# Performance work log

Hardware: AMD Instinct MI355X
Metric: run time of the kernel (lower is better)

The kernel has to match this reference:

```python
import jax, jax.numpy as jnp
import numpy as np

FS = 128; WIN = 4; C_IN = 64; C_OUT = 512; BATCH = 1024
K = FS // 4            # conv kernel = 32
STRIDE = K // 2        # 16
WS = FS * WIN          # 512 samples
T = (WS - K) // STRIDE + 1  # 31 time steps
THRESH = 1.0
BN_EPS = 1e-5

# snntorch-style spike with ATan surrogate (alpha=2): fwd Heaviside, bwd 1/(1+(pi*x)^2)
@jax.custom_vjp
def spike_fn(x):
    return (x > 0).astype(x.dtype)

def _spike_fwd(x):
    return (x > 0).astype(x.dtype), x

def _spike_bwd(x, g):
    return (g / (1.0 + (jnp.pi * x) ** 2),)

spike_fn.defvjp(_spike_fwd, _spike_bwd)

def leaky_step(inp, mem, beta):
    # snntorch Leaky, reset_mechanism='subtract': reset computed from PREVIOUS mem, detached
    reset = jax.lax.stop_gradient((mem > THRESH).astype(mem.dtype))
    mem_new = jnp.clip(beta, 0.0, 1.0) * mem + inp - reset * THRESH
    spk = spike_fn(mem_new - THRESH)
    return spk, mem_new

def setup_inputs() -> dict:
    key = jax.random.key(0)
    ks = jax.random.split(key, 10)
    return {
        "x": jax.random.normal(ks[0], (BATCH, C_IN, WS), jnp.float32),
        "conv_w": jax.random.normal(ks[1], (C_OUT, C_IN, K), jnp.float32) * (1.0 / np.sqrt(C_IN * K)),
        "conv_b": jax.random.normal(ks[2], (C_OUT,), jnp.float32) * 0.01,
        "bn_gamma": jnp.ones((C_OUT,), jnp.float32),
        "bn_beta": jnp.zeros((C_OUT,), jnp.float32),
        "bn_mean": jnp.zeros((C_OUT,), jnp.float32),
        "bn_var": jnp.ones((C_OUT,), jnp.float32),
        "fc1_w": jax.random.normal(ks[3], (C_OUT, C_OUT), jnp.float32) * (1.0 / np.sqrt(C_OUT)),
        "fc1_b": jax.random.normal(ks[4], (C_OUT,), jnp.float32) * 0.01,
        "fc2_w": jax.random.normal(ks[5], (2, C_OUT), jnp.float32) * (1.0 / np.sqrt(C_OUT)),
        "fc2_b": jax.random.normal(ks[6], (2,), jnp.float32) * 0.01,
        "beta_enc": jax.random.uniform(ks[7], (C_OUT,), jnp.float32),
        "beta_hid": jax.random.uniform(ks[8], (C_OUT,), jnp.float32),
        "beta_out": jax.random.uniform(ks[9], (2,), jnp.float32),
    }

def reference(x, conv_w, conv_b, bn_gamma, bn_beta, bn_mean, bn_var,
              fc1_w, fc1_b, fc2_w, fc2_b, beta_enc, beta_hid, beta_out):
    # Conv1d: x [B, C_in, WS] -> [B, C_out, T]
    out = jax.lax.conv_general_dilated(
        x, conv_w, window_strides=(STRIDE,), padding='VALID',
        dimension_numbers=('NCH', 'OIH', 'NCH')) + conv_b[None, :, None]
    # BatchNorm1d (eval mode with running stats); dropout is identity in eval
    inv = jax.lax.rsqrt(bn_var + BN_EPS)
    out = bn_gamma[None, :, None] * (out - bn_mean[None, :, None]) * inv[None, :, None] + bn_beta[None, :, None]
    seq = jnp.transpose(out, (2, 0, 1))  # [T, B, C_out]

    mems0 = (jnp.zeros((BATCH, C_OUT), out.dtype),
             jnp.zeros((BATCH, C_OUT), out.dtype),
             jnp.zeros((BATCH, 2), out.dtype))

    def step(carry, xt):
        em, hm, om = carry
        spk_e, em = leaky_step(xt, em, beta_enc)
        cur1 = spk_e @ fc1_w.T + fc1_b
        spk_h, hm = leaky_step(cur1, hm, beta_hid)
        cur2 = spk_h @ fc2_w.T + fc2_b
        spk_o, om = leaky_step(cur2, om, beta_out)
        return (em, hm, om), (spk_o, om)

    (em, hm, om), (spk_rec, mem_rec) = jax.lax.scan(step, mems0, seq)
    return om, spk_rec, mem_rec
```

## Files before the change

### kernel.cpp

```cpp
#include <hip/hip_runtime.h>

#define T_STEPS 31
#define CIN     64
#define COUT    512
#define WSLEN   512
#define CSTRIDE 16
#define KRED    2048
#define NBATCH  1024
#define BCHUNK  512
#define MCHUNK  (BCHUNK * T_STEPS)
#define NMT     (MCHUNK / 16)

typedef int v4i __attribute__((ext_vector_type(4)));

__device__ __forceinline__ double clip01d(double v) { return fmin(fmax(v, 0.0), 1.0); }

__device__ __forceinline__ void gl_lds16(const void* g, void* l) {
    __builtin_amdgcn_global_load_lds(
        (const __attribute__((address_space(1))) void*)g,
        (__attribute__((address_space(3))) void*)l, 16, 0, 0);
}

__device__ __forceinline__ void dig5(float4 f, unsigned int w[5]) {
    float vv[4] = {f.x, f.y, f.z, f.w};
    unsigned int w0 = 0, w1 = 0, w2 = 0, w3 = 0, w4 = 0;
    #pragma unroll
    for (int e = 0; e < 4; ++e) {
        float v  = vv[e];
        float c0 = rintf(v * 16384.0f);
        float r1 = fmaf(c0, -6.103515625e-05f, v);
        float c1 = rintf(r1 * 268435456.0f);
        float r2 = fmaf(c1, -3.725290298461914e-09f, r1);
        float c2 = rintf(r2 * 34359738368.0f);
        int i0 = (int)c0, i1 = (int)c1, i2 = (int)c2;
        int d2 = ((i0 + 64) & 127) - 64;
        int d1 = (i0 - d2) >> 7;
        int d4 = ((i1 + 64) & 127) - 64;
        int d3 = (i1 - d4) >> 7;
        w0 |= (unsigned int)(d1 & 255) << (8 * e);
        w1 |= (unsigned int)(d2 & 255) << (8 * e);
        w2 |= (unsigned int)(d3 & 255) << (8 * e);
        w3 |= (unsigned int)(d4 & 255) << (8 * e);
        w4 |= (unsigned int)(i2 & 255) << (8 * e);
    }
    w[0] = w0; w[1] = w1; w[2] = w2; w[3] = w3; w[4] = w4;
}

__global__ __launch_bounds__(256) void prep_digits_kernel(
    const float* __restrict__ conv_w, const float* __restrict__ fc1_w,
    signed char* __restrict__ Bd, signed char* __restrict__ Fd)
{
    int t = blockIdx.x * 256 + threadIdx.x;
    if (t < 262144) {
        int k4 = (t & 511) << 2;
        int co = t >> 9;
        float4 w4 = *(const float4*)(conv_w + (size_t)co * KRED + k4);
        float4 v4 = make_float4(w4.x * 4.0f, w4.y * 4.0f, w4.z * 4.0f, w4.w * 4.0f);
        unsigned int pk[5];
        dig5(v4, pk);
        int off = (((k4 >> 6) * 32 + (co >> 4)) << 10)
                + ((co & 15) + ((k4 >> 4) & 3) * 16) * 16 + (k4 & 15);
        #pragma unroll
        for (int q = 0; q < 5; ++q)
            *(unsigned int*)(Bd + q * 1048576 + off) = pk[q];
    } else {
        int u  = t - 262144;
        int k4 = (u & 127) << 2;
        int co = u >> 7;
        float4 w4 = *(const float4*)(fc1_w + (size_t)co * COUT + k4);
        float4 v4 = make_float4(w4.x * 4.0f, w4.y * 4.0f, w4.z * 4.0f, w4.w * 4.0f);
        unsigned int pk[5];
        dig5(v4, pk);
        int off = (((k4 >> 6) * 32 + (co >> 4)) << 10)
                + ((co & 15) + ((k4 >> 4) & 3) * 16) * 16 + (k4 & 15);
        #pragma unroll
        for (int q = 0; q < 5; ++q)
            *(unsigned int*)(Fd + q * 262144 + off) = pk[q];
    }
}

__global__ __launch_bounds__(512) void conv_bn_i8v6_kernel(
    const float* __restrict__ x, const signed char* __restrict__ Bd,
    const float* __restrict__ conv_b,
    const float* __restrict__ bn_gamma, const float* __restrict__ bn_beta,
    const float* __restrict__ bn_mean,  const float* __restrict__ bn_var,
    double* __restrict__ seq, int b_base)
{
    __shared__ __align__(16) signed char Alds[5 * 2048];
    __shared__ __align__(16) signed char Blds[5 * 8192];

    const int tid = threadIdx.x;
    const int nMB = MCHUNK / 32;
    const int bm  = blockIdx.x % nMB;
    const int bnk = blockIdx.x / nMB;
    const int m0 = bm * 32, n0 = bnk * 128;

    const int rA  = tid & 31;
    const int gA  = tid >> 5;
    const int kqA = gA & 3;
    const int jq  = gA >> 2;
    const int mA  = m0 + rA;
    const int bA  = b_base + mA / T_STEPS;
    const int tA  = mA % T_STEPS;
    const float* xp = x + (size_t)bA * CIN * WSLEN + tA * CSTRIDE;
    const int awb  = ((rA >> 4) << 10) + ((rA & 15) + kqA * 16) * 16 + jq * 4;
    const int kloc = kqA * 16 + jq * 4;

    const int wv  = tid >> 6;
    const int l   = tid & 63;
    const int rgM = wv >> 2;
    const int cw  = wv & 3;

    v4i acc[2][5];
    #pragma unroll
    for (int s = 0; s < 2; ++s)
        #pragma unroll
        for (int d = 0; d < 5; ++d) acc[s][d] = (v4i){0, 0, 0, 0};

    float4 sxa = *(const float4*)(xp + (kloc >> 5) * WSLEN + (kloc & 31));

    for (int kt = 0; kt < 32; ++kt) {
        unsigned int pa[5];
        dig5(make_float4(sxa.x * 0.125f, sxa.y * 0.125f, sxa.z * 0.125f, sxa.w * 0.125f), pa);

        __syncthreads();
        #pragma unroll
        for (int p = 0; p < 5; ++p)
            *(unsigned int*)(Alds + p * 2048 + awb) = pa[p];

        #pragma unroll
        for (int i = 0; i < 5; ++i) {
            const int s   = wv * 5 + i;
            const int q   = s >> 3;
            const int ctl = s & 7;
            const signed char* gsrc = Bd + (size_t)q * 1048576
                + (((size_t)(kt * 32 + bnk * 8 + ctl)) << 10) + l * 16;
            gl_lds16(gsrc, Blds + q * 8192 + ctl * 1024);
        }

        if (kt + 1 < 32) {
            int gk = (kt + 1) * 64 + kloc;
            sxa = *(const float4*)(xp + (gk >> 5) * WSLEN + (gk & 31));
        }
        __syncthreads();

        v4i aF[5];
        #pragma unroll
        for (int p = 0; p < 5; ++p)
            aF[p] = *(const v4i*)(Alds + p * 2048 + (rgM << 10) + (l << 4));

        #define MF(A_, B_, C_) __builtin_amdgcn_mfma_i32_16x16x64_i8(A_, B_, C_, 0, 0, 0)
        #pragma unroll
        for (int s = 0; s < 2; ++s) {
            const signed char* bb = Blds + ((cw * 2 + s) << 10) + (l << 4);
            v4i b0 = *(const v4i*)(bb);
            v4i b1 = *(const v4i*)(bb + 8192);
            v4i b2 = *(const v4i*)(bb + 16384);
            v4i b3 = *(const v4i*)(bb + 24576);
            v4i b4 = *(const v4i*)(bb + 32768);
            acc[s][0] = MF(aF[0], b0, acc[s][0]);
            acc[s][1] = MF(aF[1], b0, MF(aF[0], b1, acc[s][1]));
            acc[s][2] = MF(aF[2], b0, MF(aF[1], b1, MF(aF[0], b2, acc[s][2])));
            acc[s][3] = MF(aF[3], b0, MF(aF[2], b1, MF(aF[1], b2, MF(aF[0], b3, acc[s][3]))));
            acc[s][4] = MF(aF[4], b0, MF(aF[3], b1, MF(aF[2], b2, MF(aF[1], b3, MF(aF[0], b4, acc[s][4])))));
        }
        #undef MF
    }

    const int l15 = l & 15;
    const int rq  = l >> 4;
    #pragma unroll
    for (int s = 0; s < 2; ++s) {
        const int co = n0 + (cw * 2 + s) * 16 + l15;
        const double g   = (double)bn_gamma[co];
        const double be  = (double)bn_beta[co];
        const double mn  = (double)bn_mean[co];
        const double vr  = (double)bn_var[co];
        const double cb  = (double)conv_b[co];
        const double inv = 1.0 / sqrt(vr + 1e-5);
        #pragma unroll
        for (int r = 0; r < 4; ++r) {
            double v = (double)acc[s][0][r] * 0x1p-13
                     + (double)acc[s][1][r] * 0x1p-20
                     + (double)acc[s][2][r] * 0x1p-27
                     + (double)acc[s][3][r] * 0x1p-34
                     + (double)acc[s][4][r] * 0x1p-41;
            int m = m0 + rgM * 16 + rq * 4 + r;
            seq[(size_t)m * COUT + co] = g * (v + cb - mn) * inv + be;
        }
    }
}

__global__ __launch_bounds__(512) void enc_scan_kernel(
    const double* __restrict__ seq, const float* __restrict__ beta_enc,
    signed char* __restrict__ Sd)
{
    const int c = threadIdx.x;
    const int b = blockIdx.x;
    const double be = clip01d((double)beta_enc[c]);
    const double* sp = seq + (size_t)b * T_STEPS * COUT + c;
    const size_t cblk = (size_t)(c >> 6) * NMT;
    const int    coff = ((c >> 4) & 3) * 16;
    const int    j    = c & 15;
    double em = 0.0;
    for (int t = 0; t < T_STEPS; ++t) {
        double e = be * em + sp[(size_t)t * COUT] - ((em > 1.0) ? 1.0 : 0.0);
        em = e;
        int m = b * T_STEPS + t;
        Sd[((cblk + (m >> 4)) << 10) + ((m & 15) + coff) * 16 + j] =
            (e > 1.0) ? (signed char)1 : (signed char)0;
    }
}

__global__ __launch_bounds__(512) void fc1_gemm_kernel(
    const signed char* __restrict__ Sd, const signed char* __restrict__ Fd,
    double* __restrict__ cur1)
{
    __shared__ __align__(16) signed char AldsK[2048];
    __shared__ __align__(16) signed char BldsK[5 * 8192];

    const int tid = threadIdx.x;
    const int nMB = MCHUNK / 32;
    const int bm  = blockIdx.x % nMB;
    const int bnk = blockIdx.x / nMB;
    const int m0 = bm * 32, n0 = bnk * 128;

    const int wv  = tid >> 6;
    const int l   = tid & 63;
    const int rgM = wv >> 2;
    const int cw  = wv & 3;

    v4i acc[2][5];
    #pragma unroll
    for (int s = 0; s < 2; ++s)
        #pragma unroll
        for (int d = 0; d < 5; ++d) acc[s][d] = (v4i){0, 0, 0, 0};

    for (int kt = 0; kt < 8; ++kt) {
        __syncthreads();
        #pragma unroll
        for (int i = 0; i < 5; ++i) {
            const int s   = wv * 5 + i;
            const int q   = s >> 3;
            const int ctl = s & 7;
            const signed char* gsrc = Fd + (size_t)q * 262144
                + (((size_t)(kt * 32 + bnk * 8 + ctl)) << 10) + l * 16;
            gl_lds16(gsrc, BldsK + q * 8192 + ctl * 1024);
        }
        if (wv < 2) {
            const signed char* gsrc = Sd
                + (((size_t)(kt * NMT + bm * 2 + wv)) << 10) + l * 16;
            gl_lds16(gsrc, AldsK + wv * 1024);
        }
        __syncthreads();

        v4i aF = *(const v4i*)(AldsK + (rgM << 10) + (l << 4));
        #define MF(A_, B_, C_) __builtin_amdgcn_mfma_i32_16x16x64_i8(A_, B_, C_, 0, 0, 0)
        #pragma unroll
        for (int s = 0; s < 2; ++s) {
            const signed char* bb = BldsK + ((cw * 2 + s) << 10) + (l << 4);
            acc[s][0] = MF(aF, *(const v4i*)(bb),         acc[s][0]);
            acc[s][1] = MF(aF, *(const v4i*)(bb + 8192),  acc[s][1]);
            acc[s][2] = MF(aF, *(const v4i*)(bb + 16384), acc[s][2]);
            acc[s][3] = MF(aF, *(const v4i*)(bb + 24576), acc[s][3]);
            acc[s][4] = MF(aF, *(const v4i*)(bb + 32768), acc[s][4]);
        }
        #undef MF
    }

    const int l15 = l & 15;
    const int rq  = l >> 4;
    #pragma unroll
    for (int s = 0; s < 2; ++s) {
        const int co = n0 + (cw * 2 + s) * 16 + l15;
        #pragma unroll
        for (int r = 0; r < 4; ++r) {
            double v = (double)acc[s][0][r] * 0x1p-9
                     + (double)acc[s][1][r] * 0x1p-16
                     + (double)acc[s][2][r] * 0x1p-23
                     + (double)acc[s][3][r] * 0x1p-30
                     + (double)acc[s][4][r] * 0x1p-37;
            int m = m0 + rgM * 16 + rq * 4 + r;
            cur1[(size_t)m * COUT + co] = v;
        }
    }
}

__global__ __launch_bounds__(512, 4) void hid_out_scan_kernel(
    const double* __restrict__ cur1, const float* __restrict__ fc1_b,
    const float* __restrict__ fc2_w, const float* __restrict__ fc2_b,
    const float* __restrict__ beta_hid, const float* __restrict__ beta_out,
    float* __restrict__ out, int b_base)
{
    __shared__ double red[8][2];

    const int tid  = threadIdx.x;
    const int lane = tid & 63;
    const int wave = tid >> 6;
    const int row  = blockIdx.x;
    const int brow = b_base + row;

    const double bh  = clip01d((double)beta_hid[tid]);
    const double f1b = (double)fc1_b[tid];
    const double w2a = (double)fc2_w[tid];
    const double w2b = (double)fc2_w[COUT + tid];

    double bo = 0.0, f2b = 0.0, om = 0.0;
    if (tid < 2) { bo = clip01d((double)beta_out[tid]); f2b = (double)fc2_b[tid]; }

    double hm = 0.0;
    const double* cp = cur1 + (size_t)row * T_STEPS * COUT + tid;

    for (int t = 0; t < T_STEPS; ++t) {
        double cur = cp[(size_t)t * COUT] + f1b;
        double h = bh * hm + cur - ((hm > 1.0) ? 1.0 : 0.0);
        hm = h;
        double sh = (h > 1.0) ? 1.0 : 0.0;
        double p0 = sh * w2a;
        double p1 = sh * w2b;
        #pragma unroll
        for (int off = 32; off > 0; off >>= 1) {
            p0 += __shfl_down(p0, off);
            p1 += __shfl_down(p1, off);
        }
        if (lane == 0) { red[wave][0] = p0; red[wave][1] = p1; }
        __syncthreads();
        if (tid < 2) {
            double cur2 = f2b;
            #pragma unroll
            for (int w = 0; w < 8; ++w) cur2 += red[w][tid];
            double o = bo * om + cur2 - ((om > 1.0) ? 1.0 : 0.0);
            om = o;
            float so = (o > 1.0) ? 1.0f : 0.0f;
            int bidx = brow * 2 + tid;
            out[2048 + t * 2048 + bidx] = so;
            out[2048 + 63488 + t * 2048 + bidx] = (float)o;
            if (t == T_STEPS - 1) out[bidx] = (float)o;
        }
        __syncthreads();
    }
}

extern "C" void kernel_launch(void* const* d_in, const int* in_sizes, int n_in,
                              void* d_out, int out_size, void* d_ws, size_t ws_size,
                              hipStream_t stream)
{
    const float* x        = (const float*)d_in[0];
    const float* conv_w   = (const float*)d_in[1];
    const float* conv_b   = (const float*)d_in[2];
    const float* bn_gamma = (const float*)d_in[3];
    const float* bn_beta  = (const float*)d_in[4];
    const float* bn_mean  = (const float*)d_in[5];
    const float* bn_var   = (const float*)d_in[6];
    const float* fc1_w    = (const float*)d_in[7];
    const float* fc1_b    = (const float*)d_in[8];
    const float* fc2_w    = (const float*)d_in[9];
    const float* fc2_b    = (const float*)d_in[10];
    const float* beta_enc = (const float*)d_in[11];
    const float* beta_hid = (const float*)d_in[12];
    const float* beta_out = (const float*)d_in[13];
    float* out = (float*)d_out;

    signed char* Bd  = (signed char*)d_ws;
    signed char* Fd  = (signed char*)d_ws + 5 * 1048576;
    signed char* Sd  = (signed char*)d_ws + 7 * 1048576;
    double*      seq = (double*)((char*)d_ws + 16 * 1048576);

    prep_digits_kernel<<<1280, 256, 0, stream>>>(conv_w, fc1_w, Bd, Fd);

    for (int chunk = 0; chunk < 2; ++chunk) {
        int b_base = chunk * BCHUNK;
        conv_bn_i8v6_kernel<<<(MCHUNK / 32) * (COUT / 128), 512, 0, stream>>>(
            x, Bd, conv_b, bn_gamma, bn_beta, bn_mean, bn_var, seq, b_base);
        enc_scan_kernel<<<BCHUNK, 512, 0, stream>>>(seq, beta_enc, Sd);
        fc1_gemm_kernel<<<(MCHUNK / 32) * (COUT / 128), 512, 0, stream>>>(
            Sd, Fd, seq);
        hid_out_scan_kernel<<<BCHUNK, 512, 0, stream>>>(
            seq, fc1_b, fc2_w, fc2_b, beta_hid, beta_out, out, b_base);
    }
}
```

Measured before the change: 712.4 us.

## Predigitize input x into int8 planes before conv GEMM

```diff
diff --git a/kernel.cpp b/kernel.cpp
--- a/kernel.cpp
+++ b/kernel.cpp
@@ -10,6 +10,7 @@
 #define BCHUNK  512
 #define MCHUNK  (BCHUNK * T_STEPS)
 #define NMT     (MCHUNK / 16)
+#define XPLANE  16777216
 
 typedef int v4i __attribute__((ext_vector_type(4)));
 
@@ -79,6 +80,123 @@
     }
 }
 
+__global__ __launch_bounds__(256) void digx_kernel(
+    const float* __restrict__ x, signed char* __restrict__ Xd, int b_base)
+{
+    size_t t = (size_t)blockIdx.x * 256 + threadIdx.x;
+    size_t off4 = t * 4;
+    float4 v = *(const float4*)(x + (size_t)b_base * CIN * WSLEN + off4);
+    unsigned int pk[5];
+    dig5(make_float4(v.x * 0.125f, v.y * 0.125f, v.z * 0.125f, v.w * 0.125f), pk);
+    #pragma unroll
+    for (int p = 0; p < 5; ++p)
+        *(unsigned int*)(Xd + (size_t)p * XPLANE + off4) = pk[p];
+}
+
+__global__ __launch_bounds__(512) void conv_bn_i8v11_kernel(
+    const signed char* __restrict__ Xd, const signed char* __restrict__ Bd,
+    const float* __restrict__ conv_b,
+    const float* __restrict__ bn_gamma, const float* __restrict__ bn_beta,
+    const float* __restrict__ bn_mean,  const float* __restrict__ bn_var,
+    double* __restrict__ seq)
+{
+    __shared__ __align__(16) signed char Alds[5 * 2048];
+    __shared__ __align__(16) signed char Blds[5 * 8192];
+
+    const int tid = threadIdx.x;
+    const int nMB = MCHUNK / 32;
+    const int bm  = blockIdx.x % nMB;
+    const int bnk = blockIdx.x / nMB;
+    const int m0 = bm * 32, n0 = bnk * 128;
+
+    const int wv  = tid >> 6;
+    const int l   = tid & 63;
+    const int rgM = wv >> 2;
+    const int cw  = wv & 3;
+
+    const int rL = l & 15, qL = l >> 4;
+    const int st0 = wv & 1;
+    const int m_0 = m0 + st0 * 16 + rL;
+    const int bl0 = m_0 / T_STEPS, t_0 = m_0 % T_STEPS;
+    const signed char* srcA0 = Xd + (size_t)(wv >> 1) * XPLANE
+        + ((size_t)(bl0 * 64 + (qL >> 1)) << 9) + t_0 * 16 + (qL & 1) * 16;
+    signed char* dstA0 = Alds + (wv >> 1) * 2048 + st0 * 1024;
+    const int m_1 = m0 + (wv & 1) * 16 + rL;
+    const int bl1 = m_1 / T_STEPS, t_1 = m_1 % T_STEPS;
+    const signed char* srcA1 = Xd + (size_t)4 * XPLANE
+        + ((size_t)(bl1 * 64 + (qL >> 1)) << 9) + t_1 * 16 + (qL & 1) * 16;
+    signed char* dstA1 = Alds + 4 * 2048 + (wv & 1) * 1024;
+
+    v4i acc[2][5];
+    #pragma unroll
+    for (int s = 0; s < 2; ++s)
+        #pragma unroll
+        for (int d = 0; d < 5; ++d) acc[s][d] = (v4i){0, 0, 0, 0};
+
+    for (int kt = 0; kt < 32; ++kt) {
+        __syncthreads();
+
+        gl_lds16(srcA0 + kt * 1024, dstA0);
+        if (wv < 2) gl_lds16(srcA1 + kt * 1024, dstA1);
+
+        #pragma unroll
+        for (int i = 0; i < 5; ++i) {
+            const int s   = wv * 5 + i;
+            const int q   = s >> 3;
+            const int ctl = s & 7;
+            const signed char* gsrc = Bd + (size_t)q * 1048576
+                + (((size_t)(kt * 32 + bnk * 8 + ctl)) << 10) + l * 16;
+            gl_lds16(gsrc, Blds + q * 8192 + ctl * 1024);
+        }
+        __syncthreads();
+
+        v4i aF[5];
+        #pragma unroll
+        for (int p = 0; p < 5; ++p)
+            aF[p] = *(const v4i*)(Alds + p * 2048 + (rgM << 10) + (l << 4));
+
+        #define MF(A_, B_, C_) __builtin_amdgcn_mfma_i32_16x16x64_i8(A_, B_, C_, 0, 0, 0)
+        #pragma unroll
+        for (int s = 0; s < 2; ++s) {
+            const signed char* bb = Blds + ((cw * 2 + s) << 10) + (l << 4);
+            v4i b0 = *(const v4i*)(bb);
+            v4i b1 = *(const v4i*)(bb + 8192);
+            v4i b2 = *(const v4i*)(bb + 16384);
+            v4i b3 = *(const v4i*)(bb + 24576);
+            v4i b4 = *(const v4i*)(bb + 32768);
+            acc[s][0] = MF(aF[0], b0, acc[s][0]);
+            acc[s][1] = MF(aF[1], b0, MF(aF[0], b1, acc[s][1]));
+            acc[s][2] = MF(aF[2], b0, MF(aF[1], b1, MF(aF[0], b2, acc[s][2])));
+            acc[s][3] = MF(aF[3], b0, MF(aF[2], b1, MF(aF[1], b2, MF(aF[0], b3, acc[s][3]))));
+            acc[s][4] = MF(aF[4], b0, MF(aF[3], b1, MF(aF[2], b2, MF(aF[1], b3, MF(aF[0], b4, acc[s][4])))));
+        }
+        #undef MF
+    }
+
+    const int l15 = l & 15;
+    const int rq  = l >> 4;
+    #pragma unroll
+    for (int s = 0; s < 2; ++s) {
+        const int co = n0 + (cw * 2 + s) * 16 + l15;
+        const double g   = (double)bn_gamma[co];
+        const double be  = (double)bn_beta[co];
+        const double mn  = (double)bn_mean[co];
+        const double vr  = (double)bn_var[co];
+        const double cb  = (double)conv_b[co];
+        const double inv = 1.0 / sqrt(vr + 1e-5);
+        #pragma unroll
+        for (int r = 0; r < 4; ++r) {
+            double v = (double)acc[s][0][r] * 0x1p-13
+                     + (double)acc[s][1][r] * 0x1p-20
+                     + (double)acc[s][2][r] * 0x1p-27
+                     + (double)acc[s][3][r] * 0x1p-34
+                     + (double)acc[s][4][r] * 0x1p-41;
+            int m = m0 + rgM * 16 + rq * 4 + r;
+            seq[(size_t)m * COUT + co] = g * (v + cb - mn) * inv + be;
+        }
+    }
+}
+
 __global__ __launch_bounds__(512) void conv_bn_i8v6_kernel(
     const float* __restrict__ x, const signed char* __restrict__ Bd,
     const float* __restrict__ conv_b,
@@ -368,14 +486,30 @@
 
     prep_digits_kernel<<<1280, 256, 0, stream>>>(conv_w, fc1_w, Bd, Fd);
 
-    for (int chunk = 0; chunk < 2; ++chunk) {
-        int b_base = chunk * BCHUNK;
-        conv_bn_i8v6_kernel<<<(MCHUNK / 32) * (COUT / 128), 512, 0, stream>>>(
-            x, Bd, conv_b, bn_gamma, bn_beta, bn_mean, bn_var, seq, b_base);
-        enc_scan_kernel<<<BCHUNK, 512, 0, stream>>>(seq, beta_enc, Sd);
-        fc1_gemm_kernel<<<(MCHUNK / 32) * (COUT / 128), 512, 0, stream>>>(
-            Sd, Fd, seq);
-        hid_out_scan_kernel<<<BCHUNK, 512, 0, stream>>>(
-            seq, fc1_b, fc2_w, fc2_b, beta_hid, beta_out, out, b_base);
-    }
-}
+    const size_t NEED_XD = 160ull * 1048576;
+    if (ws_size >= NEED_XD) {
+        signed char* Xd = (signed char*)d_ws + 80ull * 1048576;
+        for (int chunk = 0; chunk < 2; ++chunk) {
+            int b_base = chunk * BCHUNK;
+            digx_kernel<<<16384, 256, 0, stream>>>(x, Xd, b_base);
+            conv_bn_i8v11_kernel<<<(MCHUNK / 32) * (COUT / 128), 512, 0, stream>>>(
+                Xd, Bd, conv_b, bn_gamma, bn_beta, bn_mean, bn_var, seq);
+            enc_scan_kernel<<<BCHUNK, 512, 0, stream>>>(seq, beta_enc, Sd);
+            fc1_gemm_kernel<<<(MCHUNK / 32) * (COUT / 128), 512, 0, stream>>>(
+                Sd, Fd, seq);
+            hid_out_scan_kernel<<<BCHUNK, 512, 0, stream>>>(
+                seq, fc1_b, fc2_w, fc2_b, beta_hid, beta_out, out, b_base);
+        }
+    } else {
+        for (int chunk = 0; chunk < 2; ++chunk) {
+            int b_base = chunk * BCHUNK;
+            conv_bn_i8v6_kernel<<<(MCHUNK / 32) * (COUT / 128), 512, 0, stream>>>(
+                x, Bd, conv_b, bn_gamma, bn_beta, bn_mean, bn_var, seq, b_base);
+            enc_scan_kernel<<<BCHUNK, 512, 0, stream>>>(seq, beta_enc, Sd);
+            fc1_gemm_kernel<<<(MCHUNK / 32) * (COUT / 128), 512, 0, stream>>>(
+                Sd, Fd, seq);
+            hid_out_scan_kernel<<<BCHUNK, 512, 0, stream>>>(
+                seq, fc1_b, fc2_w, fc2_b, beta_hid, beta_out, out, b_base);
+        }
+    }
+}
```

Result: faster. 662.3 us (median of 2 runs) (-7.0%).
